# Kernel tuning notes

Measured on AMD Instinct MI355X. Metric: run time of the kernel, lower is better.

Reference implementation:

```python
import jax, jax.numpy as jnp
import numpy as np

NUM_TOKENS = 8192
MODEL_DIM = 4096
NUM_EXPERTS = 64
CAPACITY_FACTOR = 1.0


def setup_inputs() -> dict:
    key = jax.random.key(0)
    k1, k2 = jax.random.split(key)
    inp = jax.random.normal(k1, (NUM_TOKENS, MODEL_DIM), dtype=jnp.float32)
    wg = jax.random.normal(k2, (NUM_EXPERTS, MODEL_DIM), dtype=jnp.float32) * (1.0 / np.sqrt(MODEL_DIM))
    return {"input": inp, "wg_weight": wg}


def reference(input, wg_weight):
    # logits = input @ wg.T  -> [T, E]
    logits = jnp.einsum('td,ed->te', input, wg_weight)
    num_tokens, num_experts = logits.shape
    capacity = int(CAPACITY_FACTOR * ((num_tokens + num_experts - 1) // num_experts))

    indices1_s = jnp.argmax(logits, axis=1)                      # [T]
    mask1 = jax.nn.one_hot(indices1_s, num_experts, dtype=logits.dtype)  # [T, E]
    gates = jax.nn.softmax(logits, axis=1)                       # [T, E]
    gates1_s = jnp.sum(gates * mask1, axis=1)                    # [T]

    # locations: position of each token within its chosen expert's queue
    # (exclusive cumsum over the one-hot mask, gathered at the chosen expert)
    locations1 = jnp.cumsum(mask1, axis=0) - 1.0                 # [T, E]
    locations1_s = jnp.sum(locations1 * mask1, axis=1).astype(jnp.int32)  # [T]

    # load-balancing aux loss (float32 branch of the original)
    me = jnp.sum(gates, axis=0)                                  # [E]
    ce = jnp.sum(mask1, axis=0)                                  # [E]
    l_aux = jnp.sum(me * ce) * (num_experts / (num_tokens * num_tokens))

    return (l_aux, indices1_s.astype(jnp.int32), locations1_s, gates1_s)
```

## Files before the change

kernel.cpp:

```cpp
#include <hip/hip_runtime.h>

namespace {
constexpr int TOK = 8192;
constexpr int DIM = 4096;
constexpr int NE  = 64;
constexpr int TB  = 128;
constexpr int KS  = 8;
constexpr int KR  = DIM / KS;
constexpr int BK  = 32;
constexpr int NT  = TOK / TB;
constexpr int NITER = KR / BK;
constexpr int LSTR = 40;
constexpr int GB  = 64;
constexpr int NCH = TOK / GB;
}

typedef _Float16 f16x8 __attribute__((ext_vector_type(8)));
typedef _Float16 f16x4 __attribute__((ext_vector_type(4)));
typedef float    f32x4 __attribute__((ext_vector_type(4)));

__global__ __launch_bounds__(256) void gemm_split(
    const float* __restrict__ A, const float* __restrict__ W,
    float* __restrict__ partial) {
  __shared__ _Float16 sm[(2 * TB + 2 * NE) * LSTR];
  _Float16* sAhi = sm;
  _Float16* sAlo = sm + TB * LSTR;
  _Float16* sWhi = sm + 2 * TB * LSTR;
  _Float16* sWlo = sm + 2 * TB * LSTR + NE * LSTR;

  const int bid  = blockIdx.x;
  const int tile = bid & (NT - 1);
  const int ks   = bid / NT;
  const int t0   = tile * TB;
  const int k0   = ks * KR;
  const int tid  = threadIdx.x;
  const int w    = tid >> 6;
  const int lane = tid & 63;
  const int col  = lane & 15;
  const int quad = lane >> 4;

  float4 ra[4], rw[2];
  {
#pragma unroll
    for (int j = 0; j < 4; ++j) {
      const int f4 = tid + 256 * j;
      const int tk = f4 >> 3, kc = (f4 & 7) * 4;
      ra[j] = *(const float4*)(A + (size_t)(t0 + tk) * DIM + k0 + kc);
    }
#pragma unroll
    for (int j = 0; j < 2; ++j) {
      const int f4 = tid + 256 * j;
      const int ee = f4 >> 3, kc = (f4 & 7) * 4;
      rw[j] = *(const float4*)(W + (size_t)ee * DIM + k0 + kc);
    }
  }

  f32x4 acc[2][4];
#pragma unroll
  for (int i = 0; i < 2; ++i)
#pragma unroll
    for (int j = 0; j < 4; ++j) acc[i][j] = (f32x4)0.0f;

  for (int it = 0; it < NITER; ++it) {
    __syncthreads();
#pragma unroll
    for (int j = 0; j < 4; ++j) {
      const int f4 = tid + 256 * j;
      const int tk = f4 >> 3, kc = (f4 & 7) * 4;
      const float4 r = ra[j];
      const _Float16 hx = (_Float16)r.x, hy = (_Float16)r.y,
                     hz = (_Float16)r.z, hw = (_Float16)r.w;
      *(f16x4*)(sAhi + tk * LSTR + kc) = (f16x4){hx, hy, hz, hw};
      *(f16x4*)(sAlo + tk * LSTR + kc) =
          (f16x4){(_Float16)(r.x - (float)hx), (_Float16)(r.y - (float)hy),
                  (_Float16)(r.z - (float)hz), (_Float16)(r.w - (float)hw)};
    }
#pragma unroll
    for (int j = 0; j < 2; ++j) {
      const int f4 = tid + 256 * j;
      const int ee = f4 >> 3, kc = (f4 & 7) * 4;
      const float4 r = rw[j];
      const _Float16 hx = (_Float16)r.x, hy = (_Float16)r.y,
                     hz = (_Float16)r.z, hw = (_Float16)r.w;
      *(f16x4*)(sWhi + ee * LSTR + kc) = (f16x4){hx, hy, hz, hw};
      *(f16x4*)(sWlo + ee * LSTR + kc) =
          (f16x4){(_Float16)(r.x - (float)hx), (_Float16)(r.y - (float)hy),
                  (_Float16)(r.z - (float)hz), (_Float16)(r.w - (float)hw)};
    }
    __syncthreads();
    if (it + 1 < NITER) {
      const int kb = k0 + (it + 1) * BK;
#pragma unroll
      for (int j = 0; j < 4; ++j) {
        const int f4 = tid + 256 * j;
        const int tk = f4 >> 3, kc = (f4 & 7) * 4;
        ra[j] = *(const float4*)(A + (size_t)(t0 + tk) * DIM + kb + kc);
      }
#pragma unroll
      for (int j = 0; j < 2; ++j) {
        const int f4 = tid + 256 * j;
        const int ee = f4 >> 3, kc = (f4 & 7) * 4;
        rw[j] = *(const float4*)(W + (size_t)ee * DIM + kb + kc);
      }
    }
    f16x8 ah[2], al[2], bh[4], bl[4];
#pragma unroll
    for (int mt = 0; mt < 2; ++mt) {
      const int r = w * 32 + mt * 16 + col;
      ah[mt] = *(const f16x8*)(sAhi + r * LSTR + quad * 8);
      al[mt] = *(const f16x8*)(sAlo + r * LSTR + quad * 8);
    }
#pragma unroll
    for (int et = 0; et < 4; ++et) {
      const int e = et * 16 + col;
      bh[et] = *(const f16x8*)(sWhi + e * LSTR + quad * 8);
      bl[et] = *(const f16x8*)(sWlo + e * LSTR + quad * 8);
    }
#pragma unroll
    for (int mt = 0; mt < 2; ++mt)
#pragma unroll
      for (int et = 0; et < 4; ++et) {
        acc[mt][et] = __builtin_amdgcn_mfma_f32_16x16x32_f16(
            ah[mt], bh[et], acc[mt][et], 0, 0, 0);
        acc[mt][et] = __builtin_amdgcn_mfma_f32_16x16x32_f16(
            ah[mt], bl[et], acc[mt][et], 0, 0, 0);
        acc[mt][et] = __builtin_amdgcn_mfma_f32_16x16x32_f16(
            al[mt], bh[et], acc[mt][et], 0, 0, 0);
      }
  }

  float* P = partial + (size_t)ks * TOK * NE;
#pragma unroll
  for (int mt = 0; mt < 2; ++mt)
#pragma unroll
    for (int et = 0; et < 4; ++et) {
      const int e = et * 16 + col;
#pragma unroll
      for (int r = 0; r < 4; ++r) {
        const int t = t0 + w * 32 + mt * 16 + quad * 4 + r;
        P[(size_t)t * NE + e] = acc[mt][et][r];
      }
    }
}

__global__ __launch_bounds__(256) void gating(
    const float* __restrict__ partial, float* __restrict__ out,
    int* __restrict__ idx_int, int* __restrict__ rankp,
    int* __restrict__ hist, float* __restrict__ me_part) {
  __shared__ float L[GB * 65];
  __shared__ float mx[GB];
  __shared__ float dninv[GB];
  __shared__ int   eid[GB];
  const int b = blockIdx.x, tid = threadIdx.x;
  const size_t base = (size_t)b * GB * NE;

#pragma unroll
  for (int j = 0; j < (GB * NE) / 256; ++j) {
    const int idx = tid + 256 * j;
    float s = 0.0f;
#pragma unroll
    for (int k = 0; k < KS; ++k)
      s += partial[(size_t)k * TOK * NE + base + idx];
    L[(idx >> 6) * 65 + (idx & 63)] = s;
  }
  __syncthreads();

  if (tid < GB) {
    const int t = tid;
    float m = -3.0e38f; int bi = 0;
    for (int e = 0; e < NE; ++e) {
      const float v = L[t * 65 + e];
      if (v > m) { m = v; bi = e; }
    }
    float s = 0.0f;
    for (int e = 0; e < NE; ++e) s += __expf(L[t * 65 + e] - m);
    const float inv = 1.0f / s;
    mx[t] = m; dninv[t] = inv; eid[t] = bi;
    const int gt = b * GB + t;
    out[1 + gt]           = (float)bi;
    out[1 + 2 * TOK + gt] = inv;
    idx_int[gt] = bi;
  }
  __syncthreads();

  if (tid < GB) {
    const int t = tid, e = eid[t];
    int r = 0;
    for (int j = 0; j < t; ++j) r += (eid[j] == e) ? 1 : 0;
    rankp[b * GB + t] = r;
    int c = 0;
    for (int t2 = 0; t2 < GB; ++t2) c += (eid[t2] == tid) ? 1 : 0;
    hist[b * NE + tid] = c;
  } else if (tid < 2 * GB) {
    const int e = tid - GB;
    float s = 0.0f;
    for (int t2 = 0; t2 < GB; ++t2)
      s += __expf(L[t2 * 65 + e] - mx[t2]) * dninv[t2];
    me_part[b * NE + e] = s;
  }
}

__global__ __launch_bounds__(256) void finalize(
    const int* __restrict__ idx_int, const int* __restrict__ rankp,
    const int* __restrict__ hist, const float* __restrict__ me_part,
    float* __restrict__ out) {
  __shared__ int   H[NCH * NE];
  __shared__ int   SEG[4 * NE];
  __shared__ float MEp[4 * NE];
  __shared__ float CE[NE];
  const int tid = threadIdx.x;
  const int e = tid & 63, seg = tid >> 6;

  for (int j = tid; j < NCH * NE; j += 256) H[j] = hist[j];
  {
    float s = 0.0f;
    for (int c = seg * 32; c < seg * 32 + 32; ++c) s += me_part[c * NE + e];
    MEp[seg * NE + e] = s;
  }
  __syncthreads();
  {
    int hs = 0;
    for (int c = seg * 32; c < seg * 32 + 32; ++c) hs += H[c * NE + e];
    SEG[seg * NE + e] = hs;
  }
  __syncthreads();
  if (tid < NE) {
    int run = 0;
    for (int s2 = 0; s2 < 4; ++s2) {
      const int v = SEG[s2 * NE + tid];
      SEG[s2 * NE + tid] = run;
      run += v;
    }
    CE[tid] = (float)run;
  }
  __syncthreads();
  {
    int run = SEG[seg * NE + e];
    for (int c = seg * 32; c < seg * 32 + 32; ++c) {
      const int v = H[c * NE + e];
      H[c * NE + e] = run;
      run += v;
    }
  }
  if (tid < 64) {
    float p = (MEp[tid] + MEp[NE + tid] + MEp[2 * NE + tid] + MEp[3 * NE + tid])
              * CE[tid];
#pragma unroll
    for (int off = 32; off > 0; off >>= 1) p += __shfl_down(p, off);
    if (tid == 0) out[0] = p * ((float)NE / ((float)TOK * (float)TOK));
  }
  __syncthreads();
#pragma unroll 4
  for (int i = tid; i < TOK; i += 256) {
    const int ex = idx_int[i];
    out[1 + TOK + i] = (float)(H[(i >> 6) * NE + ex] + rankp[i]);
  }
}

extern "C" void kernel_launch(void* const* d_in, const int* in_sizes, int n_in,
                              void* d_out, int out_size, void* d_ws, size_t ws_size,
                              hipStream_t stream) {
  const float* A = (const float*)d_in[0];
  const float* W = (const float*)d_in[1];
  float* out = (float*)d_out;
  char* ws = (char*)d_ws;

  float* partial = (float*)ws;
  const size_t poff = (size_t)KS * TOK * NE * sizeof(float);
  float* me_part = (float*)(ws + poff);
  int*  idx_int = (int*)(ws + poff + NCH * NE * sizeof(float));
  int*  rankp   = idx_int + TOK;
  int*  hist    = rankp + TOK;

  hipLaunchKernelGGL(gemm_split, dim3(NT * KS), dim3(256), 0, stream, A, W, partial);
  hipLaunchKernelGGL(gating, dim3(NCH), dim3(256), 0, stream, partial, out,
                     idx_int, rankp, hist, me_part);
  hipLaunchKernelGGL(finalize, dim3(1), dim3(256), 0, stream, idx_int, rankp,
                     hist, me_part, out);
}
```

Before: 212.0 us.

## Prepack W into MFMA-fragment fp16 hi/lo layout and drop LDS staging in GEMM

A new prepass kernel splits W into fp16 hi/lo halves once per call and stores them in the exact per-lane MFMA fragment order. The GEMM then loads W fragments straight from global memory and loads A directly into registers per wave, so LDS staging and the __syncthreads barriers go away. Each wave now owns 16 tokens with 512-thread blocks, in place of 32 tokens per wave with 256-thread blocks. The aim is to cut the LDS traffic, barrier stalls and repeated W conversion. The cost is an extra kernel launch and W fragments re-read from global/L2 by every wave.

```diff
diff --git a/kernel.cpp b/kernel.cpp
--- a/kernel.cpp
+++ b/kernel.cpp
@@ -7,140 +7,101 @@
 constexpr int TB  = 128;
 constexpr int KS  = 8;
 constexpr int KR  = DIM / KS;
-constexpr int BK  = 32;
+constexpr int NKS = KR / 32;
+constexpr int TOTKS = DIM / 32;
 constexpr int NT  = TOK / TB;
-constexpr int NITER = KR / BK;
-constexpr int LSTR = 40;
 constexpr int GB  = 64;
 constexpr int NCH = TOK / GB;
 }
 
 typedef _Float16 f16x8 __attribute__((ext_vector_type(8)));
-typedef _Float16 f16x4 __attribute__((ext_vector_type(4)));
 typedef float    f32x4 __attribute__((ext_vector_type(4)));
 
-__global__ __launch_bounds__(256) void gemm_split(
-    const float* __restrict__ A, const float* __restrict__ W,
-    float* __restrict__ partial) {
-  __shared__ _Float16 sm[(2 * TB + 2 * NE) * LSTR];
-  _Float16* sAhi = sm;
-  _Float16* sAlo = sm + TB * LSTR;
-  _Float16* sWhi = sm + 2 * TB * LSTR;
-  _Float16* sWlo = sm + 2 * TB * LSTR + NE * LSTR;
-
+__global__ __launch_bounds__(256) void prepack_w(
+    const float* __restrict__ W, f16x8* __restrict__ whi,
+    f16x8* __restrict__ wlo) {
+  const int gid = blockIdx.x * 256 + threadIdx.x;
+  const int lane = gid & 63;
+  const int gk   = (gid >> 6) & (TOTKS - 1);
+  const int et   = gid >> 13;
+  const int e = et * 16 + (lane & 15);
+  const int k = gk * 32 + (lane >> 4) * 8;
+  const float4 r0 = *(const float4*)(W + (size_t)e * DIM + k);
+  const float4 r1 = *(const float4*)(W + (size_t)e * DIM + k + 4);
+  f16x8 hi, lo;
+  const float rv[8] = {r0.x, r0.y, r0.z, r0.w, r1.x, r1.y, r1.z, r1.w};
+#pragma unroll
+  for (int j = 0; j < 8; ++j) {
+    const _Float16 h = (_Float16)rv[j];
+    hi[j] = h;
+    lo[j] = (_Float16)(rv[j] - (float)h);
+  }
+  whi[gid] = hi;
+  wlo[gid] = lo;
+}
+
+__global__ __launch_bounds__(512, 4) void gemm_split(
+    const float* __restrict__ A, const f16x8* __restrict__ whi,
+    const f16x8* __restrict__ wlo, float* __restrict__ partial) {
   const int bid  = blockIdx.x;
   const int tile = bid & (NT - 1);
   const int ks   = bid / NT;
   const int t0   = tile * TB;
-  const int k0   = ks * KR;
   const int tid  = threadIdx.x;
   const int w    = tid >> 6;
   const int lane = tid & 63;
   const int col  = lane & 15;
   const int quad = lane >> 4;
 
-  float4 ra[4], rw[2];
-  {
-#pragma unroll
-    for (int j = 0; j < 4; ++j) {
-      const int f4 = tid + 256 * j;
-      const int tk = f4 >> 3, kc = (f4 & 7) * 4;
-      ra[j] = *(const float4*)(A + (size_t)(t0 + tk) * DIM + k0 + kc);
-    }
-#pragma unroll
-    for (int j = 0; j < 2; ++j) {
-      const int f4 = tid + 256 * j;
-      const int ee = f4 >> 3, kc = (f4 & 7) * 4;
-      rw[j] = *(const float4*)(W + (size_t)ee * DIM + k0 + kc);
-    }
-  }
-
-  f32x4 acc[2][4];
-#pragma unroll
-  for (int i = 0; i < 2; ++i)
-#pragma unroll
-    for (int j = 0; j < 4; ++j) acc[i][j] = (f32x4)0.0f;
-
-  for (int it = 0; it < NITER; ++it) {
-    __syncthreads();
-#pragma unroll
-    for (int j = 0; j < 4; ++j) {
-      const int f4 = tid + 256 * j;
-      const int tk = f4 >> 3, kc = (f4 & 7) * 4;
-      const float4 r = ra[j];
-      const _Float16 hx = (_Float16)r.x, hy = (_Float16)r.y,
-                     hz = (_Float16)r.z, hw = (_Float16)r.w;
-      *(f16x4*)(sAhi + tk * LSTR + kc) = (f16x4){hx, hy, hz, hw};
-      *(f16x4*)(sAlo + tk * LSTR + kc) =
-          (f16x4){(_Float16)(r.x - (float)hx), (_Float16)(r.y - (float)hy),
-                  (_Float16)(r.z - (float)hz), (_Float16)(r.w - (float)hw)};
-    }
-#pragma unroll
-    for (int j = 0; j < 2; ++j) {
-      const int f4 = tid + 256 * j;
-      const int ee = f4 >> 3, kc = (f4 & 7) * 4;
-      const float4 r = rw[j];
-      const _Float16 hx = (_Float16)r.x, hy = (_Float16)r.y,
-                     hz = (_Float16)r.z, hw = (_Float16)r.w;
-      *(f16x4*)(sWhi + ee * LSTR + kc) = (f16x4){hx, hy, hz, hw};
-      *(f16x4*)(sWlo + ee * LSTR + kc) =
-          (f16x4){(_Float16)(r.x - (float)hx), (_Float16)(r.y - (float)hy),
-                  (_Float16)(r.z - (float)hz), (_Float16)(r.w - (float)hw)};
-    }
-    __syncthreads();
-    if (it + 1 < NITER) {
-      const int kb = k0 + (it + 1) * BK;
-#pragma unroll
-      for (int j = 0; j < 4; ++j) {
-        const int f4 = tid + 256 * j;
-        const int tk = f4 >> 3, kc = (f4 & 7) * 4;
-        ra[j] = *(const float4*)(A + (size_t)(t0 + tk) * DIM + kb + kc);
-      }
-#pragma unroll
-      for (int j = 0; j < 2; ++j) {
-        const int f4 = tid + 256 * j;
-        const int ee = f4 >> 3, kc = (f4 & 7) * 4;
-        rw[j] = *(const float4*)(W + (size_t)ee * DIM + kb + kc);
-      }
-    }
-    f16x8 ah[2], al[2], bh[4], bl[4];
-#pragma unroll
-    for (int mt = 0; mt < 2; ++mt) {
-      const int r = w * 32 + mt * 16 + col;
-      ah[mt] = *(const f16x8*)(sAhi + r * LSTR + quad * 8);
-      al[mt] = *(const f16x8*)(sAlo + r * LSTR + quad * 8);
-    }
+  const float* Ap = A + (size_t)(t0 + w * 16 + col) * DIM + ks * KR + quad * 8;
+  const int gk0 = ks * NKS;
+
+  f32x4 acc[4];
+#pragma unroll
+  for (int et = 0; et < 4; ++et) acc[et] = (f32x4)0.0f;
+
+  float4 a0 = *(const float4*)(Ap);
+  float4 a1 = *(const float4*)(Ap + 4);
+
+  for (int it = 0; it < NKS; ++it) {
+    f16x8 bh[4], bl[4];
 #pragma unroll
     for (int et = 0; et < 4; ++et) {
-      const int e = et * 16 + col;
-      bh[et] = *(const f16x8*)(sWhi + e * LSTR + quad * 8);
-      bl[et] = *(const f16x8*)(sWlo + e * LSTR + quad * 8);
-    }
-#pragma unroll
-    for (int mt = 0; mt < 2; ++mt)
-#pragma unroll
-      for (int et = 0; et < 4; ++et) {
-        acc[mt][et] = __builtin_amdgcn_mfma_f32_16x16x32_f16(
-            ah[mt], bh[et], acc[mt][et], 0, 0, 0);
-        acc[mt][et] = __builtin_amdgcn_mfma_f32_16x16x32_f16(
-            ah[mt], bl[et], acc[mt][et], 0, 0, 0);
-        acc[mt][et] = __builtin_amdgcn_mfma_f32_16x16x32_f16(
-            al[mt], bh[et], acc[mt][et], 0, 0, 0);
-      }
+      const size_t bi = ((size_t)(et * TOTKS + gk0 + it) << 6) + lane;
+      bh[et] = whi[bi];
+      bl[et] = wlo[bi];
+    }
+    float4 a0n, a1n;
+    if (it + 1 < NKS) {
+      a0n = *(const float4*)(Ap + (it + 1) * 32);
+      a1n = *(const float4*)(Ap + (it + 1) * 32 + 4);
+    }
+    const float av[8] = {a0.x, a0.y, a0.z, a0.w, a1.x, a1.y, a1.z, a1.w};
+    f16x8 ah, al;
+#pragma unroll
+    for (int j = 0; j < 8; ++j) {
+      const _Float16 h = (_Float16)av[j];
+      ah[j] = h;
+      al[j] = (_Float16)(av[j] - (float)h);
+    }
+#pragma unroll
+    for (int et = 0; et < 4; ++et) {
+      acc[et] = __builtin_amdgcn_mfma_f32_16x16x32_f16(ah, bh[et], acc[et], 0, 0, 0);
+      acc[et] = __builtin_amdgcn_mfma_f32_16x16x32_f16(ah, bl[et], acc[et], 0, 0, 0);
+      acc[et] = __builtin_amdgcn_mfma_f32_16x16x32_f16(al, bh[et], acc[et], 0, 0, 0);
+    }
+    a0 = a0n; a1 = a1n;
   }
 
   float* P = partial + (size_t)ks * TOK * NE;
-#pragma unroll
-  for (int mt = 0; mt < 2; ++mt)
-#pragma unroll
-    for (int et = 0; et < 4; ++et) {
-      const int e = et * 16 + col;
-#pragma unroll
-      for (int r = 0; r < 4; ++r) {
-        const int t = t0 + w * 32 + mt * 16 + quad * 4 + r;
-        P[(size_t)t * NE + e] = acc[mt][et][r];
-      }
-    }
+  const int tb = t0 + w * 16 + quad * 4;
+#pragma unroll
+  for (int et = 0; et < 4; ++et) {
+    const int e = et * 16 + col;
+#pragma unroll
+    for (int r = 0; r < 4; ++r)
+      P[(size_t)(tb + r) * NE + e] = acc[et][r];
+  }
 }
 
 __global__ __launch_bounds__(256) void gating(
@@ -266,13 +227,17 @@
   char* ws = (char*)d_ws;
 
   float* partial = (float*)ws;
-  const size_t poff = (size_t)KS * TOK * NE * sizeof(float);
-  float* me_part = (float*)(ws + poff);
-  int*  idx_int = (int*)(ws + poff + NCH * NE * sizeof(float));
-  int*  rankp   = idx_int + TOK;
-  int*  hist    = rankp + TOK;
-
-  hipLaunchKernelGGL(gemm_split, dim3(NT * KS), dim3(256), 0, stream, A, W, partial);
+  size_t off = (size_t)KS * TOK * NE * sizeof(float);
+  f16x8* whi = (f16x8*)(ws + off);  off += (size_t)4 * TOTKS * 64 * 16;
+  f16x8* wlo = (f16x8*)(ws + off);  off += (size_t)4 * TOTKS * 64 * 16;
+  float* me_part = (float*)(ws + off);  off += (size_t)NCH * NE * sizeof(float);
+  int* idx_int = (int*)(ws + off);      off += (size_t)TOK * sizeof(int);
+  int* rankp   = (int*)(ws + off);      off += (size_t)TOK * sizeof(int);
+  int* hist    = (int*)(ws + off);
+
+  hipLaunchKernelGGL(prepack_w, dim3(128), dim3(256), 0, stream, W, whi, wlo);
+  hipLaunchKernelGGL(gemm_split, dim3(NT * KS), dim3(512), 0, stream,
+                     A, whi, wlo, partial);
   hipLaunchKernelGGL(gating, dim3(NCH), dim3(256), 0, stream, partial, out,
                      idx_int, rankp, hist, me_part);
   hipLaunchKernelGGL(finalize, dim3(1), dim3(256), 0, stream, idx_int, rankp,
```

New measurement: 222.0 us. +4.7%, slower.
